# Kernel tuning notes

Measured on AMD Instinct MI355X. Metric: run time of the kernel, lower is better.

Reference implementation:

```python
import jax, jax.numpy as jnp
import numpy as np

NUM_ATOMS = 100
D = 32        # initial_atom_dim
H = 16        # hidden_dim (multiplicity per irrep)
NB = 16       # edge_dim / number of bessel basis functions
CUT = 6.0     # radius_cutoff
DEG = 4.0     # degree_norm
OUT = 1       # output_dim
INV4PI = 1.0 / np.sqrt(4.0 * np.pi)  # 'integral' SH normalization


def _bessel(d, nb, cut):
    # e3nn soft_one_hot_linspace(basis='bessel', cutoff=True) * sqrt(nb)
    x = d[:, None]
    n = jnp.arange(1, nb + 1, dtype=d.dtype)
    safe = jnp.maximum(x, 1e-9)
    out = np.sqrt(2.0 / cut) * jnp.sin(n * jnp.pi * x / cut) / safe
    return out * (x < cut) * np.sqrt(float(nb))


def _fc(x, w1, w2):
    # e3nn FullyConnectedNet: fan-in normalized linear layers, silu, no bias
    h = jax.nn.silu(x @ w1 / np.sqrt(x.shape[-1]))
    return h @ w2 / np.sqrt(w1.shape[-1])


def _forward(atomic_numbers, edge_index, coords, atom_emb,
             fc0_w1, fc0_w2, fc1_w1, fc1_w2, w_readout):
    src, dst = edge_index[0], edge_index[1]
    N = coords.shape[0]
    E = src.shape[0]

    vec = coords[src] - coords[dst]                      # [E,3]
    dist = jnp.linalg.norm(vec, axis=-1)                 # [E]
    unit = vec / jnp.maximum(dist, 1e-9)[:, None]

    # spherical harmonics, l=0 and l=1, 'integral' normalization
    y0 = jnp.full((E,), INV4PI, dtype=coords.dtype)      # [E]
    y1 = (np.sqrt(3.0) * INV4PI) * unit                  # [E,3]
    basis = _bessel(dist, NB, CUT)                       # [E,NB]

    x = atom_emb[atomic_numbers]                         # [N,D] (row 0 is padding)

    # ---- layer 0: scalars (D x0e) x (1x0e+1x1o) -> H x0e + H x1o ----
    w = _fc(basis, fc0_w1, fc0_w2)                       # [E, 2*D*H] per-edge TP weights
    wa = w[:, : D * H].reshape(E, D, H)
    wb = w[:, D * H:].reshape(E, D, H)
    xs = x[src]
    n0 = 1.0 / np.sqrt(D)                                # path fan-in norm
    m0 = jnp.einsum('ed,edh->eh', xs, wa) * y0[:, None] * n0          # [E,H]
    m1 = jnp.einsum('ed,edh->eh', xs, wb)[:, :, None] * y1[:, None, :] * n0  # [E,H,3]
    z0 = jax.ops.segment_sum(m0, dst, num_segments=N) / DEG           # [N,H]
    z1 = jax.ops.segment_sum(m1, dst, num_segments=N) / DEG           # [N,H,3]

    # ---- layer 1: (H x0e + H x1o) x (1x0e+1x1o) -> same irreps, skip-connected ----
    w = _fc(basis, fc1_w1, fc1_w2)                       # [E, 4*H*H]
    w1_ = w[:, 0 * H * H:1 * H * H].reshape(E, H, H)     # 0e x 0e -> 0e
    w2_ = w[:, 1 * H * H:2 * H * H].reshape(E, H, H)     # 0e x 1o -> 1o
    w3_ = w[:, 2 * H * H:3 * H * H].reshape(E, H, H)     # 1o x 0e -> 1o
    w4_ = w[:, 3 * H * H:4 * H * H].reshape(E, H, H)     # 1o x 1o -> 0e (CG = dot/sqrt(3))
    s, v = z0[src], z1[src]
    n1 = 1.0 / np.sqrt(2 * H)                            # two paths per output irrep
    dot = jnp.einsum('ehm,em->eh', v, y1) / np.sqrt(3.0)
    o0 = (jnp.einsum('eh,ehk->ek', s, w1_) * y0[:, None]
          + jnp.einsum('eh,ehk->ek', dot, w4_)) * n1
    o1 = (jnp.einsum('eh,ehk->ek', s, w2_)[:, :, None] * y1[:, None, :]
          + jnp.einsum('ehm,ehk->ekm', v, w3_) * y0[:, None, None]) * n1
    z0 = jax.ops.segment_sum(o0, dst, num_segments=N) / DEG + z0      # skip
    z1 = jax.ops.segment_sum(o1, dst, num_segments=N) / DEG + z1

    # ---- scalar readout (o3.Linear onto 0e) + graph sum-pool ----
    node_scalar = z0 @ w_readout / np.sqrt(H)            # [N,OUT]
    return jnp.sum(node_scalar, axis=0)                  # [OUT]


def setup_inputs() -> dict:
    key = jax.random.key(0)
    ks = jax.random.split(key, 9)
    N, E = 10000, 160000
    atomic_numbers = jax.random.randint(ks[0], (N,), 0, NUM_ATOMS)
    coords = jax.random.normal(ks[1], (N, 3), dtype=jnp.float32)
    edge_index = jax.random.randint(ks[2], (2, E), 0, N)
    atom_emb = jax.random.normal(ks[3], (NUM_ATOMS, D), dtype=jnp.float32).at[0].set(0.0)
    fc0_w1 = jax.random.normal(ks[4], (NB, H), dtype=jnp.float32)
    fc0_w2 = jax.random.normal(ks[5], (H, 2 * D * H), dtype=jnp.float32)
    fc1_w1 = jax.random.normal(ks[6], (NB, H), dtype=jnp.float32)
    fc1_w2 = jax.random.normal(ks[7], (H, 4 * H * H), dtype=jnp.float32)
    w_readout = jax.random.normal(ks[8], (H, OUT), dtype=jnp.float32)
    return {"atomic_numbers": atomic_numbers, "coords": coords, "edge_index": edge_index,
            "atom_emb": atom_emb, "fc0_w1": fc0_w1, "fc0_w2": fc0_w2,
            "fc1_w1": fc1_w1, "fc1_w2": fc1_w2, "w_readout": w_readout}


def reference(atomic_numbers, coords, edge_index, atom_emb,
              fc0_w1, fc0_w2, fc1_w1, fc1_w2, w_readout):
    return _forward(atomic_numbers, edge_index, coords, atom_emb,
                    fc0_w1, fc0_w2, fc1_w1, fc1_w2, w_readout)
```

## Files before the change

### kernel.cpp

```cpp
#include <hip/hip_runtime.h>
#include <math.h>


namespace {
constexpr int   NATOMS   = 100;
constexpr float PI_F     = 3.14159265358979323846f;
constexpr float INV4PI_F = 0.28209479177387814f;
constexpr float SQRT3_F  = 1.7320508075688772f;
constexpr float CUT_F    = 6.0f;
constexpr float BASIS_C  = 2.3094010767585034f;
constexpr float N0_F     = 0.17677669529663687f;
constexpr float K0_F = INV4PI_F * N0_F * 0.0625f;
constexpr float K1_F = SQRT3_F * INV4PI_F * N0_F * 0.0625f;
constexpr float P2SC = INV4PI_F * N0_F * (1.0f / 64.0f);
}

__device__ __forceinline__ float silu_fast(float x) {
  return x / (1.0f + __expf(-x));
}

__device__ __forceinline__ float block_reduce_sum(float v) {
  #pragma unroll
  for (int o = 32; o > 0; o >>= 1) v += __shfl_down(v, o, 64);
  __shared__ float ls[8];
  int lane = threadIdx.x & 63;
  int w    = threadIdx.x >> 6;
  if (lane == 0) ls[w] = v;
  __syncthreads();
  float s = 0.f;
  if (threadIdx.x == 0) {
    int nw = (blockDim.x + 63) >> 6;
    for (int i = 0; i < nw; ++i) s += ls[i];
  }
  return s;
}

__global__ void __launch_bounds__(256)
table_kernel(const float* __restrict__ atom_emb,
             const float* __restrict__ fc0_w2,
             float* __restrict__ TI,
             float4* __restrict__ zero4,
             float* __restrict__ out,
             int NZ4) {
  int b = blockIdx.x;
  int tt = threadIdx.x;
  if (b < NATOMS) {
    int j = tt >> 4;
    int h = tt & 15;
    float s0 = 0.f, s1 = 0.f;
    #pragma unroll
    for (int d = 0; d < 32; ++d) {
      float x = atom_emb[b * 32 + d];
      s0 = fmaf(x, fc0_w2[j * 1024 + d * 16 + h], s0);
      s1 = fmaf(x, fc0_w2[j * 1024 + 512 + d * 16 + h], s1);
    }
    TI[b * 512 + j * 32 + 2 * h]     = s0;
    TI[b * 512 + j * 32 + 2 * h + 1] = s1;
    if (b == 0 && tt == 0) *out = 0.f;
  } else {
    int idx = (b - NATOMS) * 256 + tt;
    if (idx < NZ4) zero4[idx] = make_float4(0.f, 0.f, 0.f, 0.f);
  }
}

__global__ void __launch_bounds__(256)
edge_kernel(const int* __restrict__ ei,
            const float* __restrict__ coords,
            const int* __restrict__ an,
            const float* __restrict__ TI,
            const float* __restrict__ fc0_w1,
            float* __restrict__ zacc,
            int E) {
  int lane = threadIdx.x & 63;
  int g    = threadIdx.x >> 4;
  int t    = threadIdx.x & 15;
  int base = lane & 48;

  float w0c[16];
  #pragma unroll
  for (int k = 0; k < 16; ++k) w0c[k] = fc0_w1[k * 16 + t];

  const float angc = PI_F / CUT_F;
  int eA = blockIdx.x * 32 + g;
  int eB = eA + 16;
  bool vA = eA < E, vB = eB < E;
  int eAc = vA ? eA : 0, eBc = vB ? eB : 0;

  int sA = ei[eAc], dA = ei[E + eAc];
  int sB = ei[eBc], dB = ei[E + eBc];
  float sxA = coords[3 * sA + 0], syA = coords[3 * sA + 1], szA = coords[3 * sA + 2];
  float dxA = coords[3 * dA + 0], dyA = coords[3 * dA + 1], dzA = coords[3 * dA + 2];
  float sxB = coords[3 * sB + 0], syB = coords[3 * sB + 1], szB = coords[3 * sB + 2];
  float dxB = coords[3 * dB + 0], dyB = coords[3 * dB + 1], dzB = coords[3 * dB + 2];
  int aA = an[sA], aB = an[sB];

  float vxA = sxA - dxA, vyA = syA - dyA, vzA = szA - dzA;
  float vxB = sxB - dxB, vyB = syB - dyB, vzB = szB - dzB;
  float distA = sqrtf(vxA * vxA + vyA * vyA + vzA * vzA);
  float distB = sqrtf(vxB * vxB + vyB * vyB + vzB * vzB);
  float ivA = 1.0f / fmaxf(distA, 1e-9f);
  float ivB = 1.0f / fmaxf(distB, 1e-9f);
  float uxA = vxA * ivA, uyA = vyA * ivA, uzA = vzA * ivA;
  float uxB = vxB * ivB, uyB = vyB * ivB, uzB = vzB * ivB;
  float bcA = (distA < CUT_F) ? (BASIS_C * ivA) : 0.0f;
  float bcB = (distB < CUT_F) ? (BASIS_C * ivB) : 0.0f;

  float angA = angc * distA, angB = angc * distB;
  float scA = __sinf(angA), twA = 2.0f * __cosf(angA), spA = 0.f;
  float scB = __sinf(angB), twB = 2.0f * __cosf(angB), spB = 0.f;
  float a0A = 0.f, a0B = 0.f;
  #pragma unroll
  for (int k = 0; k < 16; ++k) {
    a0A = fmaf(scA, w0c[k], a0A);
    a0B = fmaf(scB, w0c[k], a0B);
    float snA = fmaf(twA, scA, -spA); spA = scA; scA = snA;
    float snB = fmaf(twB, scB, -spB); spB = scB; scB = snB;
  }
  float h0A = silu_fast(a0A * bcA * 0.25f);
  float h0B = silu_fast(a0B * bcB * 0.25f);

  const float2* tpA = (const float2*)(TI + aA * 512) + t;
  const float2* tpB = (const float2*)(TI + aB * 512) + t;
  float u0A = 0.f, u1A = 0.f, u0B = 0.f, u1B = 0.f;
  #pragma unroll
  for (int j = 0; j < 16; ++j) {
    float hjA = __shfl(h0A, base + j, 64);
    float hjB = __shfl(h0B, base + j, 64);
    float2 TA = tpA[j * 16];
    float2 TB = tpB[j * 16];
    u0A = fmaf(hjA, TA.x, u0A);
    u1A = fmaf(hjA, TA.y, u1A);
    u0B = fmaf(hjB, TB.x, u0B);
    u1B = fmaf(hjB, TB.y, u1B);
  }

  if (vA) {
    float* za = zacc + (size_t)dA * 64 + t;
    float m1 = K1_F * u1A;
    unsafeAtomicAdd(za,      K0_F * u0A);
    unsafeAtomicAdd(za + 16, m1 * uxA);
    unsafeAtomicAdd(za + 32, m1 * uyA);
    unsafeAtomicAdd(za + 48, m1 * uzA);
  }
  if (vB) {
    float* zb = zacc + (size_t)dB * 64 + t;
    float m1 = K1_F * u1B;
    unsafeAtomicAdd(zb,      K0_F * u0B);
    unsafeAtomicAdd(zb + 16, m1 * uxB);
    unsafeAtomicAdd(zb + 32, m1 * uyB);
    unsafeAtomicAdd(zb + 48, m1 * uzB);
  }
}

__global__ void __launch_bounds__(256)
edge2_kernel(const int* __restrict__ ei,
             const float* __restrict__ coords,
             const float* __restrict__ zacc,
             const float* __restrict__ fc1_w1,
             const float* __restrict__ fc1_w2,
             const float* __restrict__ w_readout,
             float* __restrict__ out,
             int N, int E) {
  __shared__ float ggs[512];
  {
    int j = threadIdx.x >> 4;
    int h = threadIdx.x & 15;
    float g1 = 0.f, g4 = 0.f;
    #pragma unroll
    for (int k = 0; k < 16; ++k) {
      float r = w_readout[k];
      g1 = fmaf(fc1_w2[j * 1024 + h * 16 + k], r, g1);
      g4 = fmaf(fc1_w2[j * 1024 + 768 + h * 16 + k], r, g4);
    }
    ggs[h * 16 + j]       = g1;
    ggs[256 + h * 16 + j] = g4;
  }
  __syncthreads();

  int lane = threadIdx.x & 63;
  int t    = lane & 15;
  int base = lane & 48;

  float g1r[16], g4r[16], w1c[16];
  #pragma unroll
  for (int k = 0; k < 16; ++k) {
    g1r[k] = ggs[t * 16 + k];
    g4r[k] = ggs[256 + t * 16 + k];
    w1c[k] = fc1_w1[k * 16 + t];
  }
  float rr = w_readout[t];

  const float angc = PI_F / CUT_F;
  int ggid = blockIdx.x * 16 + (threadIdx.x >> 4);
  int ngroups = gridDim.x * 16;

  float cr = 0.f;
  for (int n = ggid; n < N; n += ngroups) {
    cr += zacc[(size_t)n * 64 + t];
  }

  float c3 = 0.f;
  for (int e0 = ggid; e0 < E; e0 += 2 * ngroups) {
    int eA = e0;
    int eB = e0 + ngroups;
    bool vB = eB < E;
    int eBc = vB ? eB : eA;

    int sA = ei[eA],  dA = ei[E + eA];
    int sB = ei[eBc], dB = ei[E + eBc];
    float sxA = coords[3 * sA + 0], syA = coords[3 * sA + 1], szA = coords[3 * sA + 2];
    float dxA = coords[3 * dA + 0], dyA = coords[3 * dA + 1], dzA = coords[3 * dA + 2];
    float sxB = coords[3 * sB + 0], syB = coords[3 * sB + 1], szB = coords[3 * sB + 2];
    float dxB = coords[3 * dB + 0], dyB = coords[3 * dB + 1], dzB = coords[3 * dB + 2];

    size_t qa = (size_t)sA * 64;
    size_t qb = (size_t)sB * 64;
    float z0A = zacc[qa + t],      z0B = zacc[qb + t];
    float zxA = zacc[qa + 16 + t], zxB = zacc[qb + 16 + t];
    float zyA = zacc[qa + 32 + t], zyB = zacc[qb + 32 + t];
    float zzA = zacc[qa + 48 + t], zzB = zacc[qb + 48 + t];

    float vxA = sxA - dxA, vyA = syA - dyA, vzA = szA - dzA;
    float vxB = sxB - dxB, vyB = syB - dyB, vzB = szB - dzB;
    float distA = sqrtf(vxA * vxA + vyA * vyA + vzA * vzA);
    float distB = sqrtf(vxB * vxB + vyB * vyB + vzB * vzB);
    float ivA = 1.0f / fmaxf(distA, 1e-9f);
    float ivB = 1.0f / fmaxf(distB, 1e-9f);
    float uxA = vxA * ivA, uyA = vyA * ivA, uzA = vzA * ivA;
    float uxB = vxB * ivB, uyB = vyB * ivB, uzB = vzB * ivB;
    float bcA = (distA < CUT_F) ? (BASIS_C * ivA) : 0.0f;
    float bcB = (distB < CUT_F) ? (BASIS_C * ivB) : 0.0f;

    float angA = angc * distA, angB = angc * distB;
    float scA = __sinf(angA), twA = 2.0f * __cosf(angA), spA = 0.f;
    float scB = __sinf(angB), twB = 2.0f * __cosf(angB), spB = 0.f;
    float a1A = 0.f, a1B = 0.f;
    #pragma unroll
    for (int k = 0; k < 16; ++k) {
      a1A = fmaf(scA, w1c[k], a1A);
      a1B = fmaf(scB, w1c[k], a1B);
      float snA = fmaf(twA, scA, -spA); spA = scA; scA = snA;
      float snB = fmaf(twB, scB, -spB); spB = scB; scB = snB;
    }
    float h1A = silu_fast(a1A * bcA * 0.25f);
    float h1B = silu_fast(a1B * bcB * 0.25f);

    float H1A = 0.f, H4A = 0.f, H1B = 0.f, H4B = 0.f;
    #pragma unroll
    for (int k = 0; k < 16; ++k) {
      float hbA = __shfl(h1A, base + k, 64);
      float hbB = __shfl(h1B, base + k, 64);
      H1A = fmaf(g1r[k], hbA, H1A);
      H4A = fmaf(g4r[k], hbA, H4A);
      H1B = fmaf(g1r[k], hbB, H1B);
      H4B = fmaf(g4r[k], hbB, H4B);
    }

    float wA = fmaf(uxA, zxA, fmaf(uyA, zyA, uzA * zzA));
    float wB = fmaf(uxB, zxB, fmaf(uyB, zyB, uzB * zzB));
    c3 = fmaf(H1A, z0A, fmaf(H4A, wA, c3));
    if (vB) c3 = fmaf(H1B, z0B, fmaf(H4B, wB, c3));
  }

  float tot = block_reduce_sum(fmaf(c3, P2SC, 0.25f * rr * cr));
  if (threadIdx.x == 0) atomicAdd(out, tot);
}

extern "C" void kernel_launch(void* const* d_in, const int* in_sizes, int n_in,
                              void* d_out, int out_size, void* d_ws, size_t ws_size,
                              hipStream_t stream) {
  const int*   an        = (const int*)d_in[0];
  const float* coords    = (const float*)d_in[1];
  const int*   ei        = (const int*)d_in[2];
  const float* atom_emb  = (const float*)d_in[3];
  const float* fc0_w1    = (const float*)d_in[4];
  const float* fc0_w2    = (const float*)d_in[5];
  const float* fc1_w1    = (const float*)d_in[6];
  const float* fc1_w2    = (const float*)d_in[7];
  const float* w_readout = (const float*)d_in[8];

  int N = in_sizes[0];
  int E = in_sizes[2] / 2;

  float* zacc = (float*)d_ws;
  float* TI   = zacc + (size_t)N * 64;
  float* out  = (float*)d_out;

  int NZ4 = N * 16;
  int zblocks = (NZ4 + 255) / 256;
  table_kernel<<<NATOMS + zblocks, 256, 0, stream>>>(
      atom_emb, fc0_w2, TI, (float4*)zacc, out, NZ4);

  edge_kernel<<<(E + 31) / 32, 256, 0, stream>>>(
      ei, coords, an, TI, fc0_w1, zacc, E);

  edge2_kernel<<<2048, 256, 0, stream>>>(
      ei, coords, zacc, fc1_w1, fc1_w2, w_readout, out, N, E);
}
```

Baseline: 148.4 us.

## Precompute layer-1 edge weights in first edge pass and interleave node accumulator

Computes the layer-1 radial MLP and the readout-folded weights (H1, H4) together with unit vectors inside the first edge kernel and stores them per edge. The second edge kernel then only reads these buffers plus a float4 of the source node accumulator, so it no longer recomputes geometry, Bessel basis and MLP. The node accumulator layout changes from component-major to interleaved (4 per channel) to allow vectorized loads. In exchange the first kernel does more work per edge (it now builds the readout-folded weight table in every block) and writes about 144 bytes of extra intermediate data per edge, and its atomics now hit adjacent addresses.

```diff
diff --git a/kernel.cpp b/kernel.cpp
--- a/kernel.cpp
+++ b/kernel.cpp
@@ -69,16 +69,40 @@
             const int* __restrict__ an,
             const float* __restrict__ TI,
             const float* __restrict__ fc0_w1,
+            const float* __restrict__ fc1_w1,
+            const float* __restrict__ fc1_w2,
+            const float* __restrict__ w_readout,
             float* __restrict__ zacc,
+            float2* __restrict__ hbuf2,
+            float4* __restrict__ ubuf,
             int E) {
+  __shared__ float ggs[512];
+  {
+    int m = threadIdx.x >> 4;
+    int h = threadIdx.x & 15;
+    float g1 = 0.f, g4 = 0.f;
+    #pragma unroll
+    for (int k = 0; k < 16; ++k) {
+      float r = w_readout[k];
+      g1 = fmaf(fc1_w2[m * 1024 + h * 16 + k], r, g1);
+      g4 = fmaf(fc1_w2[m * 1024 + 768 + h * 16 + k], r, g4);
+    }
+    ggs[m * 16 + h]       = g1;
+    ggs[256 + m * 16 + h] = g4;
+  }
+  __syncthreads();
+
   int lane = threadIdx.x & 63;
   int g    = threadIdx.x >> 4;
   int t    = threadIdx.x & 15;
   int base = lane & 48;
 
-  float w0c[16];
-  #pragma unroll
-  for (int k = 0; k < 16; ++k) w0c[k] = fc0_w1[k * 16 + t];
+  float w0c[16], w1c[16];
+  #pragma unroll
+  for (int k = 0; k < 16; ++k) {
+    w0c[k] = fc0_w1[k * 16 + t];
+    w1c[k] = fc1_w1[k * 16 + t];
+  }
 
   const float angc = PI_F / CUT_F;
   int eA = blockIdx.x * 32 + g;
@@ -105,19 +129,28 @@
   float bcA = (distA < CUT_F) ? (BASIS_C * ivA) : 0.0f;
   float bcB = (distB < CUT_F) ? (BASIS_C * ivB) : 0.0f;
 
+  if (t == 0) {
+    if (vA) ubuf[eA] = make_float4(uxA, uyA, uzA, 0.f);
+    if (vB) ubuf[eB] = make_float4(uxB, uyB, uzB, 0.f);
+  }
+
   float angA = angc * distA, angB = angc * distB;
   float scA = __sinf(angA), twA = 2.0f * __cosf(angA), spA = 0.f;
   float scB = __sinf(angB), twB = 2.0f * __cosf(angB), spB = 0.f;
-  float a0A = 0.f, a0B = 0.f;
+  float a0A = 0.f, a1A = 0.f, a0B = 0.f, a1B = 0.f;
   #pragma unroll
   for (int k = 0; k < 16; ++k) {
     a0A = fmaf(scA, w0c[k], a0A);
+    a1A = fmaf(scA, w1c[k], a1A);
     a0B = fmaf(scB, w0c[k], a0B);
+    a1B = fmaf(scB, w1c[k], a1B);
     float snA = fmaf(twA, scA, -spA); spA = scA; scA = snA;
     float snB = fmaf(twB, scB, -spB); spB = scB; scB = snB;
   }
   float h0A = silu_fast(a0A * bcA * 0.25f);
+  float h1A = silu_fast(a1A * bcA * 0.25f);
   float h0B = silu_fast(a0B * bcB * 0.25f);
+  float h1B = silu_fast(a1B * bcB * 0.25f);
 
   const float2* tpA = (const float2*)(TI + aA * 512) + t;
   const float2* tpB = (const float2*)(TI + aB * 512) + t;
@@ -134,69 +167,55 @@
     u1B = fmaf(hjB, TB.y, u1B);
   }
 
+  float H1A = 0.f, H4A = 0.f, H1B = 0.f, H4B = 0.f;
+  #pragma unroll
+  for (int k = 0; k < 16; ++k) {
+    float hbA = __shfl(h1A, base + k, 64);
+    float hbB = __shfl(h1B, base + k, 64);
+    float G1k = ggs[k * 16 + t];
+    float G4k = ggs[256 + k * 16 + t];
+    H1A = fmaf(G1k, hbA, H1A);
+    H4A = fmaf(G4k, hbA, H4A);
+    H1B = fmaf(G1k, hbB, H1B);
+    H4B = fmaf(G4k, hbB, H4B);
+  }
+  if (vA) hbuf2[(size_t)eA * 16 + t] = make_float2(H1A, H4A);
+  if (vB) hbuf2[(size_t)eB * 16 + t] = make_float2(H1B, H4B);
+
   if (vA) {
-    float* za = zacc + (size_t)dA * 64 + t;
+    float* za = zacc + (size_t)dA * 64 + 4 * t;
     float m1 = K1_F * u1A;
-    unsafeAtomicAdd(za,      K0_F * u0A);
-    unsafeAtomicAdd(za + 16, m1 * uxA);
-    unsafeAtomicAdd(za + 32, m1 * uyA);
-    unsafeAtomicAdd(za + 48, m1 * uzA);
+    unsafeAtomicAdd(za,     K0_F * u0A);
+    unsafeAtomicAdd(za + 1, m1 * uxA);
+    unsafeAtomicAdd(za + 2, m1 * uyA);
+    unsafeAtomicAdd(za + 3, m1 * uzA);
   }
   if (vB) {
-    float* zb = zacc + (size_t)dB * 64 + t;
+    float* zb = zacc + (size_t)dB * 64 + 4 * t;
     float m1 = K1_F * u1B;
-    unsafeAtomicAdd(zb,      K0_F * u0B);
-    unsafeAtomicAdd(zb + 16, m1 * uxB);
-    unsafeAtomicAdd(zb + 32, m1 * uyB);
-    unsafeAtomicAdd(zb + 48, m1 * uzB);
+    unsafeAtomicAdd(zb,     K0_F * u0B);
+    unsafeAtomicAdd(zb + 1, m1 * uxB);
+    unsafeAtomicAdd(zb + 2, m1 * uyB);
+    unsafeAtomicAdd(zb + 3, m1 * uzB);
   }
 }
 
 __global__ void __launch_bounds__(256)
 edge2_kernel(const int* __restrict__ ei,
-             const float* __restrict__ coords,
+             const float4* __restrict__ ubuf,
+             const float2* __restrict__ hbuf2,
              const float* __restrict__ zacc,
-             const float* __restrict__ fc1_w1,
-             const float* __restrict__ fc1_w2,
              const float* __restrict__ w_readout,
              float* __restrict__ out,
              int N, int E) {
-  __shared__ float ggs[512];
-  {
-    int j = threadIdx.x >> 4;
-    int h = threadIdx.x & 15;
-    float g1 = 0.f, g4 = 0.f;
-    #pragma unroll
-    for (int k = 0; k < 16; ++k) {
-      float r = w_readout[k];
-      g1 = fmaf(fc1_w2[j * 1024 + h * 16 + k], r, g1);
-      g4 = fmaf(fc1_w2[j * 1024 + 768 + h * 16 + k], r, g4);
-    }
-    ggs[h * 16 + j]       = g1;
-    ggs[256 + h * 16 + j] = g4;
-  }
-  __syncthreads();
-
-  int lane = threadIdx.x & 63;
-  int t    = lane & 15;
-  int base = lane & 48;
-
-  float g1r[16], g4r[16], w1c[16];
-  #pragma unroll
-  for (int k = 0; k < 16; ++k) {
-    g1r[k] = ggs[t * 16 + k];
-    g4r[k] = ggs[256 + t * 16 + k];
-    w1c[k] = fc1_w1[k * 16 + t];
-  }
-  float rr = w_readout[t];
-
-  const float angc = PI_F / CUT_F;
+  int t    = threadIdx.x & 15;
   int ggid = blockIdx.x * 16 + (threadIdx.x >> 4);
   int ngroups = gridDim.x * 16;
+  float rr = w_readout[t];
 
   float cr = 0.f;
   for (int n = ggid; n < N; n += ngroups) {
-    cr += zacc[(size_t)n * 64 + t];
+    cr += zacc[(size_t)n * 64 + 4 * t];
   }
 
   float c3 = 0.f;
@@ -206,60 +225,20 @@
     bool vB = eB < E;
     int eBc = vB ? eB : eA;
 
-    int sA = ei[eA],  dA = ei[E + eA];
-    int sB = ei[eBc], dB = ei[E + eBc];
-    float sxA = coords[3 * sA + 0], syA = coords[3 * sA + 1], szA = coords[3 * sA + 2];
-    float dxA = coords[3 * dA + 0], dyA = coords[3 * dA + 1], dzA = coords[3 * dA + 2];
-    float sxB = coords[3 * sB + 0], syB = coords[3 * sB + 1], szB = coords[3 * sB + 2];
-    float dxB = coords[3 * dB + 0], dyB = coords[3 * dB + 1], dzB = coords[3 * dB + 2];
-
-    size_t qa = (size_t)sA * 64;
-    size_t qb = (size_t)sB * 64;
-    float z0A = zacc[qa + t],      z0B = zacc[qb + t];
-    float zxA = zacc[qa + 16 + t], zxB = zacc[qb + 16 + t];
-    float zyA = zacc[qa + 32 + t], zyB = zacc[qb + 32 + t];
-    float zzA = zacc[qa + 48 + t], zzB = zacc[qb + 48 + t];
-
-    float vxA = sxA - dxA, vyA = syA - dyA, vzA = szA - dzA;
-    float vxB = sxB - dxB, vyB = syB - dyB, vzB = szB - dzB;
-    float distA = sqrtf(vxA * vxA + vyA * vyA + vzA * vzA);
-    float distB = sqrtf(vxB * vxB + vyB * vyB + vzB * vzB);
-    float ivA = 1.0f / fmaxf(distA, 1e-9f);
-    float ivB = 1.0f / fmaxf(distB, 1e-9f);
-    float uxA = vxA * ivA, uyA = vyA * ivA, uzA = vzA * ivA;
-    float uxB = vxB * ivB, uyB = vyB * ivB, uzB = vzB * ivB;
-    float bcA = (distA < CUT_F) ? (BASIS_C * ivA) : 0.0f;
-    float bcB = (distB < CUT_F) ? (BASIS_C * ivB) : 0.0f;
-
-    float angA = angc * distA, angB = angc * distB;
-    float scA = __sinf(angA), twA = 2.0f * __cosf(angA), spA = 0.f;
-    float scB = __sinf(angB), twB = 2.0f * __cosf(angB), spB = 0.f;
-    float a1A = 0.f, a1B = 0.f;
-    #pragma unroll
-    for (int k = 0; k < 16; ++k) {
-      a1A = fmaf(scA, w1c[k], a1A);
-      a1B = fmaf(scB, w1c[k], a1B);
-      float snA = fmaf(twA, scA, -spA); spA = scA; scA = snA;
-      float snB = fmaf(twB, scB, -spB); spB = scB; scB = snB;
+    int sA = ei[eA], sB = ei[eBc];
+    float4 uA = ubuf[eA];
+    float4 uB = ubuf[eBc];
+    float2 hA = hbuf2[(size_t)eA * 16 + t];
+    float2 hB = hbuf2[(size_t)eBc * 16 + t];
+    float4 zA = *reinterpret_cast<const float4*>(zacc + (size_t)sA * 64 + 4 * t);
+    float4 zB = *reinterpret_cast<const float4*>(zacc + (size_t)sB * 64 + 4 * t);
+
+    float wA = fmaf(uA.x, zA.y, fmaf(uA.y, zA.z, uA.z * zA.w));
+    c3 = fmaf(hA.x, zA.x, fmaf(hA.y, wA, c3));
+    if (vB) {
+      float wB = fmaf(uB.x, zB.y, fmaf(uB.y, zB.z, uB.z * zB.w));
+      c3 = fmaf(hB.x, zB.x, fmaf(hB.y, wB, c3));
     }
-    float h1A = silu_fast(a1A * bcA * 0.25f);
-    float h1B = silu_fast(a1B * bcB * 0.25f);
-
-    float H1A = 0.f, H4A = 0.f, H1B = 0.f, H4B = 0.f;
-    #pragma unroll
-    for (int k = 0; k < 16; ++k) {
-      float hbA = __shfl(h1A, base + k, 64);
-      float hbB = __shfl(h1B, base + k, 64);
-      H1A = fmaf(g1r[k], hbA, H1A);
-      H4A = fmaf(g4r[k], hbA, H4A);
-      H1B = fmaf(g1r[k], hbB, H1B);
-      H4B = fmaf(g4r[k], hbB, H4B);
-    }
-
-    float wA = fmaf(uxA, zxA, fmaf(uyA, zyA, uzA * zzA));
-    float wB = fmaf(uxB, zxB, fmaf(uyB, zyB, uzB * zzB));
-    c3 = fmaf(H1A, z0A, fmaf(H4A, wA, c3));
-    if (vB) c3 = fmaf(H1B, z0B, fmaf(H4B, wB, c3));
   }
 
   float tot = block_reduce_sum(fmaf(c3, P2SC, 0.25f * rr * cr));
@@ -282,9 +261,11 @@
   int N = in_sizes[0];
   int E = in_sizes[2] / 2;
 
-  float* zacc = (float*)d_ws;
-  float* TI   = zacc + (size_t)N * 64;
-  float* out  = (float*)d_out;
+  float4* ubuf  = (float4*)d_ws;
+  float2* hbuf2 = (float2*)(ubuf + E);
+  float*  zacc  = (float*)(hbuf2 + (size_t)E * 16);
+  float*  TI    = zacc + (size_t)N * 64;
+  float*  out   = (float*)d_out;
 
   int NZ4 = N * 16;
   int zblocks = (NZ4 + 255) / 256;
@@ -292,8 +273,9 @@
       atom_emb, fc0_w2, TI, (float4*)zacc, out, NZ4);
 
   edge_kernel<<<(E + 31) / 32, 256, 0, stream>>>(
-      ei, coords, an, TI, fc0_w1, zacc, E);
+      ei, coords, an, TI, fc0_w1, fc1_w1, fc1_w2, w_readout,
+      zacc, hbuf2, ubuf, E);
 
   edge2_kernel<<<2048, 256, 0, stream>>>(
-      ei, coords, zacc, fc1_w1, fc1_w2, w_readout, out, N, E);
-}
+      ei, ubuf, hbuf2, zacc, w_readout, out, N, E);
+}
```

New measurement: 258.2 us. +73.9%, slower.
